# Optimization experiments

Measured on AMD Instinct MI355X. Metric: run time of the kernel, lower is better.

## Reference

```python
import jax, jax.numpy as jnp
import numpy as np

N = 100000       # nodes
E = 1_600_000    # edges (before self-loops)
NFEAT = 128
NHID = 32
HEADS = 4
HID = NHID * HEADS   # 128
NCLASS = 40
EPS = 1e-5
NEG = 0.2            # leaky_relu negative slope (GATConv default)


def setup_inputs() -> dict:
    key = jax.random.key(0)
    ks = jax.random.split(key, 32)
    s = 0.1
    d = {}
    d["x"] = jax.random.normal(ks[0], (N, NFEAT), jnp.float32)
    d["edge_index"] = jax.random.randint(ks[1], (2, E), 0, N, jnp.int32)
    # conv0: nfeat -> nhid, heads=4, concat
    d["W0"] = jax.random.normal(ks[2], (HID, NFEAT), jnp.float32) * s
    d["as0"] = jax.random.normal(ks[3], (HEADS, NHID), jnp.float32) * s
    d["ad0"] = jax.random.normal(ks[4], (HEADS, NHID), jnp.float32) * s
    d["b0"] = jnp.zeros((HID,), jnp.float32)
    d["g0"] = jnp.ones((HID,), jnp.float32)
    d["be0"] = jnp.zeros((HID,), jnp.float32)
    d["m0"] = jax.random.normal(ks[5], (HID,), jnp.float32) * 0.01
    d["v0"] = jax.random.uniform(ks[6], (HID,), jnp.float32, 0.5, 1.5)
    # conv1: hid -> nhid, heads=4, concat
    d["W1"] = jax.random.normal(ks[7], (HID, HID), jnp.float32) * s
    d["as1"] = jax.random.normal(ks[8], (HEADS, NHID), jnp.float32) * s
    d["ad1"] = jax.random.normal(ks[9], (HEADS, NHID), jnp.float32) * s
    d["b1"] = jnp.zeros((HID,), jnp.float32)
    d["g1"] = jnp.ones((HID,), jnp.float32)
    d["be1"] = jnp.zeros((HID,), jnp.float32)
    d["m1"] = jax.random.normal(ks[10], (HID,), jnp.float32) * 0.01
    d["v1"] = jax.random.uniform(ks[11], (HID,), jnp.float32, 0.5, 1.5)
    # conv_out: hid -> nclass, heads=1, concat=False
    d["W2"] = jax.random.normal(ks[12], (NCLASS, HID), jnp.float32) * s
    d["as2"] = jax.random.normal(ks[13], (1, NCLASS), jnp.float32) * s
    d["ad2"] = jax.random.normal(ks[14], (1, NCLASS), jnp.float32) * s
    d["b2"] = jnp.zeros((NCLASS,), jnp.float32)
    return d


def _gat(x, W, a_s, a_d, bias, src, dst, n, concat):
    # PyG GATConv: project, per-head attention logits, segment softmax over dst, scatter-sum
    H, C = a_s.shape
    h = (x @ W.T).reshape(n, H, C)                      # [N,H,C]
    al_s = jnp.einsum('nhc,hc->nh', h, a_s)             # [N,H]
    al_d = jnp.einsum('nhc,hc->nh', h, a_d)
    e = al_s[src] + al_d[dst]                           # [E,H]
    e = jnp.where(e > 0, e, NEG * e)                    # leaky_relu
    m = jax.ops.segment_max(e, dst, num_segments=n)     # self-loops guarantee nonempty segments
    ex = jnp.exp(e - m[dst])
    ssum = jax.ops.segment_sum(ex, dst, num_segments=n)
    alpha = ex / ssum[dst]                              # [E,H]
    out = jax.ops.segment_sum(alpha[:, :, None] * h[src], dst, num_segments=n)  # [N,H,C]
    out = out.reshape(n, H * C) if concat else out.mean(axis=1)
    return out + bias


def _bn_eval(x, g, b, m, v):
    return (x - m) * jax.lax.rsqrt(v + EPS) * g + b


def reference(x, edge_index, W0, as0, ad0, b0, g0, be0, m0, v0,
              W1, as1, ad1, b1, g1, be1, m1, v1, W2, as2, ad2, b2):
    n = x.shape[0]
    loop = jnp.arange(n, dtype=edge_index.dtype)
    src = jnp.concatenate([edge_index[0], loop])        # add_self_loops=True (PyG default)
    dst = jnp.concatenate([edge_index[1], loop])
    h = _gat(x, W0, as0, ad0, b0, src, dst, n, True)
    h = jax.nn.relu(_bn_eval(h, g0, be0, m0, v0))       # dropout is identity in eval
    h = _gat(h, W1, as1, ad1, b1, src, dst, n, True)
    h = jax.nn.relu(_bn_eval(h, g1, be1, m1, v1))
    h = _gat(h, W2, as2, ad2, b2, src, dst, n, False)
    return jax.nn.log_softmax(h, axis=1)
```

## Files before the change

### kernel.cpp

```cpp
#include <hip/hip_runtime.h>
#include <math.h>

#define NEGS 0.2f
#define EPSBN 1e-5f
#define NBIN_MAX 256
#define SBITS 9
#define SNODES 512
#define GLH 256

typedef __attribute__((ext_vector_type(8))) short short8v;
typedef __attribute__((ext_vector_type(4))) float f32x4;

static __device__ __forceinline__ float lrelu(float x){ return x > 0.f ? x : NEGS*x; }
static __device__ __forceinline__ float bf_lo(unsigned u){ return __uint_as_float(u << 16); }
static __device__ __forceinline__ float bf_hi(unsigned u){ return __uint_as_float(u & 0xffff0000u); }
static __device__ __forceinline__ float bf1(unsigned short v){ return __uint_as_float(((unsigned)v) << 16); }
static __device__ __forceinline__ unsigned short f2bf(float f){
  unsigned u = __float_as_uint(f);
  unsigned r = (u + 0x7fff + ((u >> 16) & 1)) >> 16;
  return (unsigned short)r;
}

__global__ void k_padW2(const float* __restrict__ W2, float* __restrict__ Wt2p){
  int i = blockIdx.x*256 + threadIdx.x;
  if (i >= 128*64) return;
  int k = i >> 6, c = i & 63;
  Wt2p[i] = (c < 40) ? W2[c*128 + k] : 0.f;
}

__global__ void k_deg(const int* __restrict__ ei, int E, int N, int* __restrict__ deg){
  int i = blockIdx.x*256 + threadIdx.x;
  if (i >= E + N) return;
  int d = (i < E) ? ei[E + i] : (i - E);
  atomicAdd(&deg[d], 1);
}

__global__ void k_scan1(const int* __restrict__ deg, int* __restrict__ incl,
                        int* __restrict__ partials, int n){
  __shared__ int sd[256];
  int tid = threadIdx.x;
  int base = blockIdx.x*1024 + tid*4;
  int v[4]; int s = 0;
  #pragma unroll
  for (int j=0;j<4;++j){ int idx = base+j; v[j] = (idx<n)? deg[idx] : 0; s += v[j]; }
  sd[tid] = s; __syncthreads();
  for (int off=1; off<256; off<<=1){
    int t = (tid>=off)? sd[tid-off] : 0;
    __syncthreads();
    sd[tid] += t;
    __syncthreads();
  }
  int run = sd[tid] - s;
  #pragma unroll
  for (int j=0;j<4;++j){ int idx = base+j; run += v[j]; if (idx<n) incl[idx] = run; }
  if (tid==255) partials[blockIdx.x] = sd[255];
}

__global__ void k_scan2(int* partials, int nb){
  __shared__ int sd[256];
  int tid = threadIdx.x;
  sd[tid] = (tid<nb)? partials[tid] : 0;
  __syncthreads();
  for (int off=1; off<256; off<<=1){
    int t = (tid>=off)? sd[tid-off] : 0;
    __syncthreads();
    sd[tid] += t;
    __syncthreads();
  }
  if (tid<nb) partials[tid] = sd[tid];
}

__global__ void k_scan3(int* __restrict__ offs, const int* __restrict__ partials, int n){
  int i = blockIdx.x*256 + threadIdx.x;
  if (i == 0) offs[0] = 0;
  if (i >= n) return;
  int b = i >> 10;
  if (b > 0) offs[i+1] += partials[b-1];
}

__global__ __launch_bounds__(256) void k_lhist(const int* __restrict__ ei, int E, int N,
                                               int* __restrict__ Hmat, int nbin){
  __shared__ int lh[NBIN_MAX];
  int tid = threadIdx.x;
  lh[tid] = 0;
  __syncthreads();
  int ET = E + N;
  int c0 = (int)(((long long)ET * blockIdx.x) / GLH);
  int c1 = (int)(((long long)ET * (blockIdx.x+1)) / GLH);
  for (int i = c0 + tid; i < c1; i += 256){
    int d = (i < E) ? ei[E + i] : (i - E);
    atomicAdd(&lh[d >> SBITS], 1);
  }
  __syncthreads();
  for (int b = tid; b < nbin; b += 256)
    Hmat[b*GLH + blockIdx.x] = lh[b];
}

__global__ __launch_bounds__(256) void k_write(const int* __restrict__ ei, int E, int N,
                        const int* __restrict__ Bmat, uint2* __restrict__ staged, int nbin){
  __shared__ int cur[NBIN_MAX];
  int tid = threadIdx.x;
  for (int b = tid; b < nbin; b += 256)
    cur[b] = Bmat[b*GLH + blockIdx.x];
  __syncthreads();
  int ET = E + N;
  int c0 = (int)(((long long)ET * blockIdx.x) / GLH);
  int c1 = (int)(((long long)ET * (blockIdx.x+1)) / GLH);
  for (int i = c0 + tid; i < c1; i += 256){
    int s, d;
    if (i < E){ s = ei[i]; d = ei[E+i]; } else { s = i-E; d = i-E; }
    int pos = atomicAdd(&cur[d >> SBITS], 1);
    staged[pos] = make_uint2((unsigned)s, (unsigned)d);
  }
}

__global__ __launch_bounds__(256) void k_bucket2(const uint2* __restrict__ staged,
                         const int* __restrict__ offs, int* __restrict__ csr, int N){
  __shared__ int scur[SNODES];
  int b = blockIdx.x, tid = threadIdx.x;
  int node0 = b << SBITS;
  int nn = min(SNODES, N - node0);
  if (tid < nn) scur[tid] = offs[node0 + tid];
  if (tid + 256 < nn) scur[tid + 256] = offs[node0 + tid + 256];
  __syncthreads();
  int base = offs[node0];
  int endp = offs[node0 + nn];
  for (int e = base + tid; e < endp; e += 256){
    uint2 p = staged[e];
    int pos = atomicAdd(&scur[p.y - node0], 1);
    csr[pos] = (int)p.x;
  }
}

template<bool BF16IN>
__global__ __launch_bounds__(256) void k_gemm128m(const void* __restrict__ Xin,
                          const float* __restrict__ W,
                          const float* __restrict__ as_, const float* __restrict__ ad_,
                          unsigned short* __restrict__ Yb,
                          float* __restrict__ ALs, float* __restrict__ ALd, int n){
  __shared__ short lds[24576];
  unsigned* ldsW = (unsigned*)lds;
  unsigned* ldsX = (unsigned*)(lds + 16384);
  int tid = threadIdx.x;
  int r0 = blockIdx.x*64;
  #pragma unroll
  for (int j=0;j<16;++j){
    int i = (256*j + tid)*4;
    int row = i >> 7;
    float4 v = *(const float4*)(W + i);
    int dw = i >> 1, lo = dw & 63, base = dw & ~63;
    int sw = base | (lo ^ ((row&7)<<2));
    uint2 p;
    p.x = (unsigned)f2bf(v.x) | ((unsigned)f2bf(v.y)<<16);
    p.y = (unsigned)f2bf(v.z) | ((unsigned)f2bf(v.w)<<16);
    *(uint2*)(&ldsW[sw]) = p;
  }
  if (!BF16IN){
    const float* X = (const float*)Xin;
    #pragma unroll
    for (int j=0;j<8;++j){
      int i = (256*j + tid)*4;
      int row = i >> 7;
      int grow = r0 + row;
      float4 v = (grow < n) ? *(const float4*)(X + (size_t)grow*128 + (i&127))
                            : make_float4(0.f,0.f,0.f,0.f);
      int dw = i >> 1, lo = dw & 63, base = dw & ~63;
      int sw = base | (lo ^ ((row&7)<<2));
      uint2 p;
      p.x = (unsigned)f2bf(v.x) | ((unsigned)f2bf(v.y)<<16);
      p.y = (unsigned)f2bf(v.z) | ((unsigned)f2bf(v.w)<<16);
      *(uint2*)(&ldsX[sw]) = p;
    }
  } else {
    const unsigned short* Xb = (const unsigned short*)Xin;
    #pragma unroll
    for (int j=0;j<4;++j){
      int dw4 = 1024*j + tid*4;
      int row = dw4 >> 6;
      int grow = r0 + row;
      uint4 v = (grow < n) ? *(const uint4*)(Xb + (size_t)grow*128 + (dw4&63)*2)
                           : make_uint4(0,0,0,0);
      int lo = dw4 & 63, base = dw4 & ~63;
      int sw = base | (lo ^ ((row&7)<<2));
      *(uint4*)(&ldsX[sw]) = v;
    }
  }
  __syncthreads();
  int l = tid & 63, w = tid >> 6;
  int lrow = l & 15, lk = l >> 4;
  int arow = w*16 + lrow;
  int abase = arow*64, ax = (arow&7)<<2;
  short8v a[4];
  #pragma unroll
  for (int ks=0;ks<4;++ks){
    int lo = ks*16 + lk*4;
    a[ks] = *(const short8v*)&ldsX[abase + (lo ^ ax)];
  }
  f32x4 acc[8];
  #pragma unroll
  for (int c=0;c<8;++c) acc[c] = (f32x4){0.f,0.f,0.f,0.f};
  #pragma unroll
  for (int c=0;c<8;++c){
    int brow = c*16 + lrow;
    int bbase2 = brow*64, bx = (brow&7)<<2;
    #pragma unroll
    for (int ks=0;ks<4;++ks){
      int lo = ks*16 + lk*4;
      short8v bfr = *(const short8v*)&ldsW[bbase2 + (lo ^ bx)];
      acc[c] = __builtin_amdgcn_mfma_f32_16x16x32_bf16(a[ks], bfr, acc[c], 0, 0, 0);
    }
  }
  __syncthreads();
  unsigned short* Ys = (unsigned short*)ldsX;
  #pragma unroll
  for (int c=0;c<8;++c){
    #pragma unroll
    for (int r=0;r<4;++r){
      int row = w*16 + lk*4 + r;
      Ys[row*128 + c*16 + lrow] = f2bf(acc[c][r]);
    }
  }
  __syncthreads();
  #pragma unroll
  for (int j=0;j<4;++j){
    int dw4 = 1024*j + tid*4;
    int row = dw4 >> 6;
    int grow = r0 + row;
    if (grow < n)
      *(uint4*)(Yb + (size_t)grow*128 + (dw4&63)*2) = *(const uint4*)&((unsigned*)ldsX)[dw4];
  }
  {
    int row = tid >> 2, h = tid & 3;
    int grow = r0 + row;
    if (grow < n){
      const unsigned short* yr = Ys + row*128 + h*32;
      float ps = 0.f, pd = 0.f;
      #pragma unroll
      for (int j=0;j<32;++j){
        float y = bf1(yr[j]);
        ps = fmaf(y, as_[h*32+j], ps);
        pd = fmaf(y, ad_[h*32+j], pd);
      }
      ALs[grow*4+h] = ps; ALd[grow*4+h] = pd;
    }
  }
}

__global__ __launch_bounds__(256) void k_agg128b(const unsigned short* __restrict__ Pb,
                         const float* __restrict__ ALs, const float* __restrict__ ALd,
                         const int* __restrict__ offs, const int* __restrict__ csr,
                         const float* __restrict__ bias, const float* __restrict__ gam,
                         const float* __restrict__ bet, const float* __restrict__ mean,
                         const float* __restrict__ var, unsigned short* __restrict__ outb, int n){
  int node = blockIdx.x*4 + (threadIdx.x >> 6);
  int lane = threadIdx.x & 63;
  if (node >= n) return;
  int el = lane >> 4, fl = lane & 15, hd = fl >> 2;
  int beg = offs[node], end = offs[node+1];
  int deg = end - beg;
  float aldh = ALd[node*4 + hd];
  int c = (lane < deg) ? csr[beg + lane] : 0;
  float a0=0.f,a1=0.f,a2=0.f,a3=0.f,a4=0.f,a5=0.f,a6=0.f,a7=0.f;
  float wsum = 0.f;
  int nsteps = (deg + 3) >> 2;
  int sCur = __shfl(c, el);
  bool vCur = el < deg;
  uint4 hvCur = *(const uint4*)(Pb + (size_t)sCur*128 + fl*8);
  float alsCur = ALs[sCur*4 + hd];
  for (int t = 0; t < nsteps; ++t){
    int idxN = 4*(t+1) + el;
    int sN = 0; float alsN = 0.f;
    uint4 hvN = make_uint4(0,0,0,0);
    if (t+1 < nsteps){
      sN = (idxN < 64) ? __shfl(c, idxN) : ((idxN < deg) ? csr[beg + idxN] : 0);
      hvN = *(const uint4*)(Pb + (size_t)sN*128 + fl*8);
      alsN = ALs[sN*4 + hd];
    }
    float w = vCur ? __expf(lrelu(alsCur + aldh)) : 0.f;
    wsum += w;
    a0 = fmaf(w, bf_lo(hvCur.x), a0);  a1 = fmaf(w, bf_hi(hvCur.x), a1);
    a2 = fmaf(w, bf_lo(hvCur.y), a2);  a3 = fmaf(w, bf_hi(hvCur.y), a3);
    a4 = fmaf(w, bf_lo(hvCur.z), a4);  a5 = fmaf(w, bf_hi(hvCur.z), a5);
    a6 = fmaf(w, bf_lo(hvCur.w), a6);  a7 = fmaf(w, bf_hi(hvCur.w), a7);
    sCur = sN; hvCur = hvN; alsCur = alsN; vCur = idxN < deg;
  }
  #pragma unroll
  for (int off=16; off<64; off<<=1){
    a0 += __shfl_xor(a0, off); a1 += __shfl_xor(a1, off);
    a2 += __shfl_xor(a2, off); a3 += __shfl_xor(a3, off);
    a4 += __shfl_xor(a4, off); a5 += __shfl_xor(a5, off);
    a6 += __shfl_xor(a6, off); a7 += __shfl_xor(a7, off);
    wsum += __shfl_xor(wsum, off);
  }
  if (el == 0){
    float inv = 1.f / wsum;
    int cc = fl*8;
    float4 bA = *(const float4*)(bias+cc), bB = *(const float4*)(bias+cc+4);
    float4 gA = *(const float4*)(gam+cc),  gB = *(const float4*)(gam+cc+4);
    float4 eA = *(const float4*)(bet+cc),  eB = *(const float4*)(bet+cc+4);
    float4 uA = *(const float4*)(mean+cc), uB = *(const float4*)(mean+cc+4);
    float4 vA = *(const float4*)(var+cc),  vB = *(const float4*)(var+cc+4);
    float o0 = (a0*inv + bA.x - uA.x) * rsqrtf(vA.x + EPSBN) * gA.x + eA.x;
    float o1 = (a1*inv + bA.y - uA.y) * rsqrtf(vA.y + EPSBN) * gA.y + eA.y;
    float o2 = (a2*inv + bA.z - uA.z) * rsqrtf(vA.z + EPSBN) * gA.z + eA.z;
    float o3 = (a3*inv + bA.w - uA.w) * rsqrtf(vA.w + EPSBN) * gA.w + eA.w;
    float o4 = (a4*inv + bB.x - uB.x) * rsqrtf(vB.x + EPSBN) * gB.x + eB.x;
    float o5 = (a5*inv + bB.y - uB.y) * rsqrtf(vB.y + EPSBN) * gB.y + eB.y;
    float o6 = (a6*inv + bB.z - uB.z) * rsqrtf(vB.z + EPSBN) * gB.z + eB.z;
    float o7 = (a7*inv + bB.w - uB.w) * rsqrtf(vB.w + EPSBN) * gB.w + eB.w;
    uint4 q;
    q.x = (unsigned)f2bf(fmaxf(o0,0.f)) | ((unsigned)f2bf(fmaxf(o1,0.f))<<16);
    q.y = (unsigned)f2bf(fmaxf(o2,0.f)) | ((unsigned)f2bf(fmaxf(o3,0.f))<<16);
    q.z = (unsigned)f2bf(fmaxf(o4,0.f)) | ((unsigned)f2bf(fmaxf(o5,0.f))<<16);
    q.w = (unsigned)f2bf(fmaxf(o6,0.f)) | ((unsigned)f2bf(fmaxf(o7,0.f))<<16);
    *(uint4*)(outb + (size_t)node*128 + cc) = q;
  }
}

__global__ __launch_bounds__(256) void k_gemm40n(const unsigned short* __restrict__ Gb,
                                                 const float* __restrict__ Wt2p,
                                                 const float* __restrict__ as2,
                                                 const float* __restrict__ ad2,
                                                 unsigned short* __restrict__ H2b,
                                                 float* __restrict__ al2s,
                                                 float* __restrict__ al2d, int n){
  __shared__ float xt[128*68];
  int tid = threadIdx.x;
  int r0 = blockIdx.x * 64;
  {
    int r  = tid & 63;
    int c0 = (tid >> 6) * 32;
    int row = r0 + r;
    #pragma unroll
    for (int j=0;j<4;++j){
      uint4 v = (row < n) ? *(const uint4*)(Gb + (size_t)row*128 + c0 + j*8)
                          : make_uint4(0,0,0,0);
      int k = c0 + j*8;
      xt[(k+0)*68 + r] = bf_lo(v.x);  xt[(k+1)*68 + r] = bf_hi(v.x);
      xt[(k+2)*68 + r] = bf_lo(v.y);  xt[(k+3)*68 + r] = bf_hi(v.y);
      xt[(k+4)*68 + r] = bf_lo(v.z);  xt[(k+5)*68 + r] = bf_hi(v.z);
      xt[(k+6)*68 + r] = bf_lo(v.w);  xt[(k+7)*68 + r] = bf_hi(v.w);
    }
  }
  __syncthreads();
  int tc = tid & 15, tr = tid >> 4;
  float acc[4][4] = {};
  #pragma unroll 4
  for (int k=0;k<128;++k){
    float4 wv = *(const float4*)(Wt2p + k*64 + tc*4);
    float4 xv = *(const float4*)(&xt[k*68 + tr*4]);
    float xv4[4] = {xv.x, xv.y, xv.z, xv.w};
    float wv4[4] = {wv.x, wv.y, wv.z, wv.w};
    #pragma unroll
    for (int u=0;u<4;++u)
      #pragma unroll
      for (int v=0;v<4;++v)
        acc[u][v] = fmaf(xv4[u], wv4[v], acc[u][v]);
  }
  float4 a4 = make_float4(0.f,0.f,0.f,0.f), d4 = a4;
  if (tc < 10){
    a4 = *(const float4*)(as2 + tc*4);
    d4 = *(const float4*)(ad2 + tc*4);
  }
  #pragma unroll
  for (int u=0;u<4;++u){
    int row = r0 + tr*4 + u;
    float ps = acc[u][0]*a4.x + acc[u][1]*a4.y + acc[u][2]*a4.z + acc[u][3]*a4.w;
    float pd = acc[u][0]*d4.x + acc[u][1]*d4.y + acc[u][2]*d4.z + acc[u][3]*d4.w;
    #pragma unroll
    for (int m=1; m<16; m<<=1){ ps += __shfl_xor(ps,m); pd += __shfl_xor(pd,m); }
    if (row < n){
      if (tc < 10){
        ushort4 o;
        o.x = f2bf(acc[u][0]); o.y = f2bf(acc[u][1]);
        o.z = f2bf(acc[u][2]); o.w = f2bf(acc[u][3]);
        *(ushort4*)(H2b + (size_t)row*40 + tc*4) = o;
      }
      if (tc == 0){ al2s[row] = ps; al2d[row] = pd; }
    }
  }
}

__global__ __launch_bounds__(256) void k_agg40b(const unsigned short* __restrict__ H2b,
                        const float* __restrict__ ALs, const float* __restrict__ ALd,
                        const int* __restrict__ offs, const int* __restrict__ csr,
                        const float* __restrict__ b2, float* __restrict__ out, int n){
  int node = blockIdx.x*4 + (threadIdx.x >> 6);
  int lane = threadIdx.x & 63;
  if (node >= n) return;
  int el = lane >> 3, fl = lane & 7;
  bool act = fl < 5;
  int beg = offs[node], end = offs[node+1];
  int deg = end - beg;
  float ald = ALd[node];
  int c = (lane < deg) ? csr[beg + lane] : 0;
  float a0=0.f,a1=0.f,a2=0.f,a3=0.f,a4=0.f,a5=0.f,a6=0.f,a7=0.f;
  float wsum = 0.f;
  int nsteps = (deg + 7) >> 3;
  int sCur = __shfl(c, el);
  bool vCur = el < deg;
  uint4 hvCur = act ? *(const uint4*)(H2b + (size_t)sCur*40 + fl*8) : make_uint4(0,0,0,0);
  float alsCur = ALs[sCur];
  for (int t = 0; t < nsteps; ++t){
    int idxN = 8*(t+1) + el;
    int sN = 0; float alsN = 0.f;
    uint4 hvN = make_uint4(0,0,0,0);
    if (t+1 < nsteps){
      sN = (idxN < 64) ? __shfl(c, idxN) : ((idxN < deg) ? csr[beg + idxN] : 0);
      if (act) hvN = *(const uint4*)(H2b + (size_t)sN*40 + fl*8);
      alsN = ALs[sN];
    }
    float w = vCur ? __expf(lrelu(alsCur + ald)) : 0.f;
    wsum += w;
    a0 = fmaf(w, bf_lo(hvCur.x), a0);  a1 = fmaf(w, bf_hi(hvCur.x), a1);
    a2 = fmaf(w, bf_lo(hvCur.y), a2);  a3 = fmaf(w, bf_hi(hvCur.y), a3);
    a4 = fmaf(w, bf_lo(hvCur.z), a4);  a5 = fmaf(w, bf_hi(hvCur.z), a5);
    a6 = fmaf(w, bf_lo(hvCur.w), a6);  a7 = fmaf(w, bf_hi(hvCur.w), a7);
    sCur = sN; hvCur = hvN; alsCur = alsN; vCur = idxN < deg;
  }
  #pragma unroll
  for (int off=8; off<64; off<<=1){
    a0 += __shfl_xor(a0, off); a1 += __shfl_xor(a1, off);
    a2 += __shfl_xor(a2, off); a3 += __shfl_xor(a3, off);
    a4 += __shfl_xor(a4, off); a5 += __shfl_xor(a5, off);
    a6 += __shfl_xor(a6, off); a7 += __shfl_xor(a7, off);
    wsum += __shfl_xor(wsum, off);
  }
  if (el == 0){
    float inv = 1.f / wsum;
    float y0=0.f,y1=0.f,y2=0.f,y3=0.f,y4=0.f,y5=0.f,y6=0.f,y7=0.f;
    if (act){
      int cc = fl*8;
      float4 bA = *(const float4*)(b2 + cc), bB = *(const float4*)(b2 + cc + 4);
      y0 = a0*inv + bA.x; y1 = a1*inv + bA.y; y2 = a2*inv + bA.z; y3 = a3*inv + bA.w;
      y4 = a4*inv + bB.x; y5 = a5*inv + bB.y; y6 = a6*inv + bB.z; y7 = a7*inv + bB.w;
    }
    float lm = act ? fmaxf(fmaxf(fmaxf(y0,y1),fmaxf(y2,y3)),
                           fmaxf(fmaxf(y4,y5),fmaxf(y6,y7))) : -1e30f;
    lm = fmaxf(lm, __shfl_xor(lm,1));
    lm = fmaxf(lm, __shfl_xor(lm,2));
    lm = fmaxf(lm, __shfl_xor(lm,4));
    float ls = act ? (__expf(y0-lm)+__expf(y1-lm)+__expf(y2-lm)+__expf(y3-lm)
                     +__expf(y4-lm)+__expf(y5-lm)+__expf(y6-lm)+__expf(y7-lm)) : 0.f;
    ls += __shfl_xor(ls,1);
    ls += __shfl_xor(ls,2);
    ls += __shfl_xor(ls,4);
    float lg = lm + __logf(ls);
    if (act){
      float4* dst = (float4*)(out + (size_t)node*40 + fl*8);
      dst[0] = make_float4(y0-lg, y1-lg, y2-lg, y3-lg);
      dst[1] = make_float4(y4-lg, y5-lg, y6-lg, y7-lg);
    }
  }
}

extern "C" void kernel_launch(void* const* d_in, const int* in_sizes, int n_in,
                              void* d_out, int out_size, void* d_ws, size_t ws_size,
                              hipStream_t stream) {
  const float* x   = (const float*)d_in[0];
  const int*   ei  = (const int*)d_in[1];
  const float* W0  = (const float*)d_in[2];
  const float* as0 = (const float*)d_in[3];
  const float* ad0 = (const float*)d_in[4];
  const float* b0  = (const float*)d_in[5];
  const float* g0  = (const float*)d_in[6];
  const float* be0 = (const float*)d_in[7];
  const float* m0  = (const float*)d_in[8];
  const float* v0  = (const float*)d_in[9];
  const float* W1  = (const float*)d_in[10];
  const float* as1 = (const float*)d_in[11];
  const float* ad1 = (const float*)d_in[12];
  const float* b1  = (const float*)d_in[13];
  const float* g1  = (const float*)d_in[14];
  const float* be1 = (const float*)d_in[15];
  const float* m1  = (const float*)d_in[16];
  const float* v1  = (const float*)d_in[17];
  const float* W2  = (const float*)d_in[18];
  const float* as2 = (const float*)d_in[19];
  const float* ad2 = (const float*)d_in[20];
  const float* b2  = (const float*)d_in[21];
  float* out = (float*)d_out;

  int N = in_sizes[0] / 128;
  int E = in_sizes[1] / 2;
  int ET = E + N;
  int NBIN = (N + SNODES - 1) >> SBITS;
  int M = NBIN * GLH;

  char* p = (char*)d_ws;
  auto alloc = [&](size_t bytes)->void* {
    void* r = (void*)p;
    p += (bytes + 255) & ~size_t(255);
    return r;
  };
  float* Wt2p  = (float*)alloc((size_t)128*64*4);
  int* deg     = (int*)alloc((size_t)N*4);
  int* offs    = (int*)alloc((size_t)(N+1)*4);
  int* partials= (int*)alloc(1024*4);
  int* Hmat    = (int*)alloc((size_t)NBIN_MAX*GLH*4);
  int* Bmat    = (int*)alloc((size_t)(NBIN_MAX*GLH+1)*4);
  int* csr     = (int*)alloc((size_t)ET*4);
  uint2* staged= (uint2*)alloc((size_t)ET*8);
  unsigned short* Pb = (unsigned short*)alloc((size_t)N*128*2);
  unsigned short* Gb = (unsigned short*)alloc((size_t)N*128*2);
  float* ALs = (float*)alloc((size_t)N*4*4);
  float* ALd = (float*)alloc((size_t)N*4*4);
  unsigned short* H2b = Pb;
  float* al2s = ALs;
  float* al2d = ALd;
  if ((size_t)(p - (char*)d_ws) > ws_size) return;

  hipMemsetAsync(deg, 0, (size_t)N*4, stream);

  k_padW2<<<(128*64+255)/256, 256, 0, stream>>>(W2, Wt2p);

  int nb1 = (N + 1023) / 1024;
  k_deg<<<(ET+255)/256, 256, 0, stream>>>(ei, E, N, deg);
  k_scan1<<<nb1, 256, 0, stream>>>(deg, offs+1, partials, N);
  k_scan2<<<1, 256, 0, stream>>>(partials, nb1);
  k_scan3<<<(N+255)/256, 256, 0, stream>>>(offs, partials, N);

  k_lhist<<<GLH, 256, 0, stream>>>(ei, E, N, Hmat, NBIN);
  int nb2 = (M + 1023) / 1024;
  k_scan1<<<nb2, 256, 0, stream>>>(Hmat, Bmat+1, partials, M);
  k_scan2<<<1, 256, 0, stream>>>(partials, nb2);
  k_scan3<<<(M+255)/256, 256, 0, stream>>>(Bmat, partials, M);
  k_write<<<GLH, 256, 0, stream>>>(ei, E, N, Bmat, staged, NBIN);
  k_bucket2<<<NBIN, 256, 0, stream>>>(staged, offs, csr, N);

  int gb = (N + 63) / 64;
  k_gemm128m<false><<<gb, 256, 0, stream>>>(x, W0, as0, ad0, Pb, ALs, ALd, N);
  k_agg128b<<<(N+3)/4, 256, 0, stream>>>(Pb, ALs, ALd, offs, csr, b0, g0, be0, m0, v0, Gb, N);

  k_gemm128m<true><<<gb, 256, 0, stream>>>(Gb, W1, as1, ad1, Pb, ALs, ALd, N);
  k_agg128b<<<(N+3)/4, 256, 0, stream>>>(Pb, ALs, ALd, offs, csr, b1, g1, be1, m1, v1, Gb, N);

  k_gemm40n<<<gb, 256, 0, stream>>>(Gb, Wt2p, as2, ad2, H2b, al2s, al2d, N);
  k_agg40b<<<(N+3)/4, 256, 0, stream>>>(H2b, al2s, al2d, offs, csr, b2, out, N);
}
```

Before: 551.6 us.

## Derive CSR offsets inside bucket kernel and batch attention weights per chunk

Removes the separate global degree atomic pass, memset and three-kernel scan. Each bucket block now counts per-node degrees in shared memory, scans them locally and writes offs itself, reusing the bin offsets from Bmat. Separately, the aggregation kernels now compute 64 attention weights at once across all lanes and broadcast them with shuffles instead of each lane recomputing exp. This drops the explicit software prefetch of the next neighbor row and relies on unrolling for overlap, which risks exposing gather latency.

```diff
diff --git a/kernel.cpp b/kernel.cpp
--- a/kernel.cpp
+++ b/kernel.cpp
@@ -28,21 +28,14 @@
   Wt2p[i] = (c < 40) ? W2[c*128 + k] : 0.f;
 }
 
-__global__ void k_deg(const int* __restrict__ ei, int E, int N, int* __restrict__ deg){
-  int i = blockIdx.x*256 + threadIdx.x;
-  if (i >= E + N) return;
-  int d = (i < E) ? ei[E + i] : (i - E);
-  atomicAdd(&deg[d], 1);
-}
-
-__global__ void k_scan1(const int* __restrict__ deg, int* __restrict__ incl,
+__global__ void k_scan1(const int* __restrict__ in, int* __restrict__ incl,
                         int* __restrict__ partials, int n){
   __shared__ int sd[256];
   int tid = threadIdx.x;
   int base = blockIdx.x*1024 + tid*4;
   int v[4]; int s = 0;
   #pragma unroll
-  for (int j=0;j<4;++j){ int idx = base+j; v[j] = (idx<n)? deg[idx] : 0; s += v[j]; }
+  for (int j=0;j<4;++j){ int idx = base+j; v[j] = (idx<n)? in[idx] : 0; s += v[j]; }
   sd[tid] = s; __syncthreads();
   for (int off=1; off<256; off<<=1){
     int t = (tid>=off)? sd[tid-off] : 0;
@@ -114,22 +107,47 @@
   }
 }
 
-__global__ __launch_bounds__(256) void k_bucket2(const uint2* __restrict__ staged,
-                         const int* __restrict__ offs, int* __restrict__ csr, int N){
-  __shared__ int scur[SNODES];
+__global__ __launch_bounds__(256) void k_bucket3(const uint2* __restrict__ staged,
+                         const int* __restrict__ Bmat,
+                         int* __restrict__ offs, int* __restrict__ csr, int N, int ET){
+  __shared__ int sdeg[SNODES];
+  __shared__ int sexc[SNODES];
   int b = blockIdx.x, tid = threadIdx.x;
   int node0 = b << SBITS;
   int nn = min(SNODES, N - node0);
-  if (tid < nn) scur[tid] = offs[node0 + tid];
-  if (tid + 256 < nn) scur[tid + 256] = offs[node0 + tid + 256];
-  __syncthreads();
-  int base = offs[node0];
-  int endp = offs[node0 + nn];
-  for (int e = base + tid; e < endp; e += 256){
-    uint2 p = staged[e];
-    int pos = atomicAdd(&scur[p.y - node0], 1);
+  int base = Bmat[b*GLH];
+  int cntb = Bmat[(b+1)*GLH] - base;
+  sdeg[2*tid] = 0; sdeg[2*tid+1] = 0;
+  __syncthreads();
+  for (int e = tid; e < cntb; e += 256){
+    uint2 p = staged[base + e];
+    atomicAdd(&sdeg[p.y - node0], 1);
+  }
+  __syncthreads();
+  int v0 = sdeg[2*tid], v1 = sdeg[2*tid+1];
+  int ps = v0 + v1;
+  sexc[tid] = ps; __syncthreads();
+  for (int off=1; off<256; off<<=1){
+    int t = (tid>=off)? sexc[tid-off] : 0;
+    __syncthreads();
+    sexc[tid] += t;
+    __syncthreads();
+  }
+  int excl_pair = sexc[tid] - ps;
+  __syncthreads();
+  sexc[2*tid]   = excl_pair;
+  sexc[2*tid+1] = excl_pair + v0;
+  if (2*tid   < nn) offs[node0 + 2*tid]   = base + excl_pair;
+  if (2*tid+1 < nn) offs[node0 + 2*tid+1] = base + excl_pair + v0;
+  sdeg[2*tid] = 0; sdeg[2*tid+1] = 0;
+  __syncthreads();
+  for (int e = tid; e < cntb; e += 256){
+    uint2 p = staged[base + e];
+    int ln = p.y - node0;
+    int pos = base + sexc[ln] + atomicAdd(&sdeg[ln], 1);
     csr[pos] = (int)p.x;
   }
+  if (b == gridDim.x - 1 && tid == 0) offs[N] = ET;
 }
 
 template<bool BF16IN>
@@ -258,31 +276,30 @@
   int el = lane >> 4, fl = lane & 15, hd = fl >> 2;
   int beg = offs[node], end = offs[node+1];
   int deg = end - beg;
-  float aldh = ALd[node*4 + hd];
+  float aldw = ALd[node*4 + (lane & 3)];
   int c = (lane < deg) ? csr[beg + lane] : 0;
   float a0=0.f,a1=0.f,a2=0.f,a3=0.f,a4=0.f,a5=0.f,a6=0.f,a7=0.f;
   float wsum = 0.f;
   int nsteps = (deg + 3) >> 2;
-  int sCur = __shfl(c, el);
-  bool vCur = el < deg;
-  uint4 hvCur = *(const uint4*)(Pb + (size_t)sCur*128 + fl*8);
-  float alsCur = ALs[sCur*4 + hd];
-  for (int t = 0; t < nsteps; ++t){
-    int idxN = 4*(t+1) + el;
-    int sN = 0; float alsN = 0.f;
-    uint4 hvN = make_uint4(0,0,0,0);
-    if (t+1 < nsteps){
-      sN = (idxN < 64) ? __shfl(c, idxN) : ((idxN < deg) ? csr[beg + idxN] : 0);
-      hvN = *(const uint4*)(Pb + (size_t)sN*128 + fl*8);
-      alsN = ALs[sN*4 + hd];
-    }
-    float w = vCur ? __expf(lrelu(alsCur + aldh)) : 0.f;
+  float wch = 0.f;
+  int wbase = el*4 + hd;
+  #pragma unroll 4
+  for (int st = 0; st < nsteps; ++st){
+    if ((st & 3) == 0){
+      int we = st*4 + (lane >> 2);
+      int ws = (we < 64) ? __shfl(c, we) : ((we < deg) ? csr[beg + we] : 0);
+      float als = ALs[ws*4 + (lane & 3)];
+      wch = (we < deg) ? __expf(lrelu(als + aldw)) : 0.f;
+    }
+    int idx = st*4 + el;
+    float w = __shfl(wch, ((st & 3) << 4) + wbase);
+    int si = (idx < 64) ? __shfl(c, idx) : ((idx < deg) ? csr[beg + idx] : 0);
+    uint4 hv = *(const uint4*)(Pb + (size_t)si*128 + fl*8);
     wsum += w;
-    a0 = fmaf(w, bf_lo(hvCur.x), a0);  a1 = fmaf(w, bf_hi(hvCur.x), a1);
-    a2 = fmaf(w, bf_lo(hvCur.y), a2);  a3 = fmaf(w, bf_hi(hvCur.y), a3);
-    a4 = fmaf(w, bf_lo(hvCur.z), a4);  a5 = fmaf(w, bf_hi(hvCur.z), a5);
-    a6 = fmaf(w, bf_lo(hvCur.w), a6);  a7 = fmaf(w, bf_hi(hvCur.w), a7);
-    sCur = sN; hvCur = hvN; alsCur = alsN; vCur = idxN < deg;
+    a0 = fmaf(w, bf_lo(hv.x), a0);  a1 = fmaf(w, bf_hi(hv.x), a1);
+    a2 = fmaf(w, bf_lo(hv.y), a2);  a3 = fmaf(w, bf_hi(hv.y), a3);
+    a4 = fmaf(w, bf_lo(hv.z), a4);  a5 = fmaf(w, bf_hi(hv.z), a5);
+    a6 = fmaf(w, bf_lo(hv.w), a6);  a7 = fmaf(w, bf_hi(hv.w), a7);
   }
   #pragma unroll
   for (int off=16; off<64; off<<=1){
@@ -397,26 +414,26 @@
   float a0=0.f,a1=0.f,a2=0.f,a3=0.f,a4=0.f,a5=0.f,a6=0.f,a7=0.f;
   float wsum = 0.f;
   int nsteps = (deg + 7) >> 3;
-  int sCur = __shfl(c, el);
-  bool vCur = el < deg;
-  uint4 hvCur = act ? *(const uint4*)(H2b + (size_t)sCur*40 + fl*8) : make_uint4(0,0,0,0);
-  float alsCur = ALs[sCur];
-  for (int t = 0; t < nsteps; ++t){
-    int idxN = 8*(t+1) + el;
-    int sN = 0; float alsN = 0.f;
-    uint4 hvN = make_uint4(0,0,0,0);
-    if (t+1 < nsteps){
-      sN = (idxN < 64) ? __shfl(c, idxN) : ((idxN < deg) ? csr[beg + idxN] : 0);
-      if (act) hvN = *(const uint4*)(H2b + (size_t)sN*40 + fl*8);
-      alsN = ALs[sN];
-    }
-    float w = vCur ? __expf(lrelu(alsCur + ald)) : 0.f;
+  float wch = 0.f;
+  #pragma unroll 4
+  for (int st = 0; st < nsteps; ++st){
+    if ((st & 7) == 0){
+      int we = st*8 + lane;
+      int ws = (we < 64) ? __shfl(c, we) : ((we < deg) ? csr[beg + we] : 0);
+      float als = ALs[ws];
+      wch = (we < deg) ? __expf(lrelu(als + ald)) : 0.f;
+    }
+    int idx = st*8 + el;
+    float w = __shfl(wch, ((st & 7) << 3) + el);
+    int si = (idx < 64) ? __shfl(c, idx) : ((idx < deg) ? csr[beg + idx] : 0);
     wsum += w;
-    a0 = fmaf(w, bf_lo(hvCur.x), a0);  a1 = fmaf(w, bf_hi(hvCur.x), a1);
-    a2 = fmaf(w, bf_lo(hvCur.y), a2);  a3 = fmaf(w, bf_hi(hvCur.y), a3);
-    a4 = fmaf(w, bf_lo(hvCur.z), a4);  a5 = fmaf(w, bf_hi(hvCur.z), a5);
-    a6 = fmaf(w, bf_lo(hvCur.w), a6);  a7 = fmaf(w, bf_hi(hvCur.w), a7);
-    sCur = sN; hvCur = hvN; alsCur = alsN; vCur = idxN < deg;
+    if (act){
+      uint4 hv = *(const uint4*)(H2b + (size_t)si*40 + fl*8);
+      a0 = fmaf(w, bf_lo(hv.x), a0);  a1 = fmaf(w, bf_hi(hv.x), a1);
+      a2 = fmaf(w, bf_lo(hv.y), a2);  a3 = fmaf(w, bf_hi(hv.y), a3);
+      a4 = fmaf(w, bf_lo(hv.z), a4);  a5 = fmaf(w, bf_hi(hv.z), a5);
+      a6 = fmaf(w, bf_lo(hv.w), a6);  a7 = fmaf(w, bf_hi(hv.w), a7);
+    }
   }
   #pragma unroll
   for (int off=8; off<64; off<<=1){
@@ -494,7 +511,6 @@
     return r;
   };
   float* Wt2p  = (float*)alloc((size_t)128*64*4);
-  int* deg     = (int*)alloc((size_t)N*4);
   int* offs    = (int*)alloc((size_t)(N+1)*4);
   int* partials= (int*)alloc(1024*4);
   int* Hmat    = (int*)alloc((size_t)NBIN_MAX*GLH*4);
@@ -510,15 +526,7 @@
   float* al2d = ALd;
   if ((size_t)(p - (char*)d_ws) > ws_size) return;
 
-  hipMemsetAsync(deg, 0, (size_t)N*4, stream);
-
   k_padW2<<<(128*64+255)/256, 256, 0, stream>>>(W2, Wt2p);
-
-  int nb1 = (N + 1023) / 1024;
-  k_deg<<<(ET+255)/256, 256, 0, stream>>>(ei, E, N, deg);
-  k_scan1<<<nb1, 256, 0, stream>>>(deg, offs+1, partials, N);
-  k_scan2<<<1, 256, 0, stream>>>(partials, nb1);
-  k_scan3<<<(N+255)/256, 256, 0, stream>>>(offs, partials, N);
 
   k_lhist<<<GLH, 256, 0, stream>>>(ei, E, N, Hmat, NBIN);
   int nb2 = (M + 1023) / 1024;
@@ -526,7 +534,7 @@
   k_scan2<<<1, 256, 0, stream>>>(partials, nb2);
   k_scan3<<<(M+255)/256, 256, 0, stream>>>(Bmat, partials, M);
   k_write<<<GLH, 256, 0, stream>>>(ei, E, N, Bmat, staged, NBIN);
-  k_bucket2<<<NBIN, 256, 0, stream>>>(staged, offs, csr, N);
+  k_bucket3<<<NBIN, 256, 0, stream>>>(staged, Bmat, offs, csr, N, ET);
 
   int gb = (N + 63) / 64;
   k_gemm128m<false><<<gb, 256, 0, stream>>>(x, W0, as0, ad0, Pb, ALs, ALd, N);
```

New measurement: 498.3 us. 1.11x faster.
